# Kernel optimization log

Measured on AMD Instinct MI355X. Metric: run time of the kernel, lower is better.

Reference implementation:

```python
import jax, jax.numpy as jnp
import numpy as np

BATCH, IN, OUT = 1024, 256, 512
ALPHA = 1.0

def setup_inputs() -> dict:
    key = jax.random.key(0)
    k1, k2, k3 = jax.random.split(key, 3)
    # kaiming-uniform-ish init scale for weight, uniform bound for bias
    bound_w = 1.0 / np.sqrt(IN)
    x = jax.random.normal(k1, (BATCH, IN), dtype=jnp.float32)
    weight = jax.random.uniform(k2, (OUT, IN), dtype=jnp.float32, minval=-bound_w, maxval=bound_w)
    bias = jax.random.uniform(k3, (OUT,), dtype=jnp.float32, minval=-bound_w, maxval=bound_w)
    return {"x": x, "weight": weight, "bias": bias}

def reference(x, weight, bias):
    # assemble[b,i,o] = x[b,i] * weight[o,i]
    # this_sum[b,o]  = sum_i assemble[b,i,o]  == x @ weight.T
    this_sum = jnp.einsum('bi,oi->bo', x, weight)
    # prod over input dim of (assemble + 1)
    assemble = x[:, :, None] * weight.T[None, :, :] + 1.0  # (B, IN, OUT)
    prod = jnp.prod(assemble, axis=1)                      # (B, OUT)
    out = prod - (1.0 - ALPHA) * this_sum - 1.0 + bias
    return out
```

## Files before the change

### kernel.cpp

```cpp
#include <hip/hip_runtime.h>


#define BATCH 1024
#define IN    256
#define OUT   512

__global__ __launch_bounds__(256, 2) void product_kernel(
    const float* __restrict__ x, const float* __restrict__ w,
    const float* __restrict__ bias, float* __restrict__ out)
{
    __shared__ float4 ws4[64 * 64];

    const int tid  = threadIdx.x;
    const int wid  = tid >> 6;
    const int lane = tid & 63;
    const int sbl  = lane >> 4;
    const int l4   = lane & 15;
    const int s    = wid * 4 + sbl;

    const int o0 = blockIdx.x * 64;
    const int b0 = blockIdx.y * 16;

    const float4* x4g = (const float4*)x;
    const float4* w4g = (const float4*)w;

    #pragma unroll
    for (int it = 0; it < 16; ++it) {
        const int r = it * 4 + wid;
        ws4[r * 64 + (lane ^ ((r >> 2) & 7))] = w4g[(o0 + r) * 64 + lane];
    }
    __syncthreads();

    float4 acc[16];
    #pragma unroll
    for (int i = 0; i < 16; ++i) acc[i] = make_float4(1.0f, 1.0f, 1.0f, 1.0f);

    const int wsw = l4 & 7;
    const int wr  = 4 * l4 * 64;

    #pragma unroll 1
    for (int p = 0; p < 4; ++p) {
        const int c = 4 * s + p;

        float4 xv[16];
        #pragma unroll
        for (int i = 0; i < 16; ++i) xv[i] = x4g[(b0 + i) * 64 + c];

        const int cw = c ^ wsw;
        const float4 wv0 = ws4[wr + 0 * 64 + cw];
        const float4 wv1 = ws4[wr + 1 * 64 + cw];
        const float4 wv2 = ws4[wr + 2 * 64 + cw];
        const float4 wv3 = ws4[wr + 3 * 64 + cw];

        #pragma unroll
        for (int i = 0; i < 16; ++i) {
            acc[i].x *= __builtin_fmaf(xv[i].x, wv0.x, 1.0f);
            acc[i].y *= __builtin_fmaf(xv[i].x, wv1.x, 1.0f);
            acc[i].z *= __builtin_fmaf(xv[i].x, wv2.x, 1.0f);
            acc[i].w *= __builtin_fmaf(xv[i].x, wv3.x, 1.0f);
            acc[i].x *= __builtin_fmaf(xv[i].y, wv0.y, 1.0f);
            acc[i].y *= __builtin_fmaf(xv[i].y, wv1.y, 1.0f);
            acc[i].z *= __builtin_fmaf(xv[i].y, wv2.y, 1.0f);
            acc[i].w *= __builtin_fmaf(xv[i].y, wv3.y, 1.0f);
            acc[i].x *= __builtin_fmaf(xv[i].z, wv0.z, 1.0f);
            acc[i].y *= __builtin_fmaf(xv[i].z, wv1.z, 1.0f);
            acc[i].z *= __builtin_fmaf(xv[i].z, wv2.z, 1.0f);
            acc[i].w *= __builtin_fmaf(xv[i].z, wv3.z, 1.0f);
            acc[i].x *= __builtin_fmaf(xv[i].w, wv0.w, 1.0f);
            acc[i].y *= __builtin_fmaf(xv[i].w, wv1.w, 1.0f);
            acc[i].z *= __builtin_fmaf(xv[i].w, wv2.w, 1.0f);
            acc[i].w *= __builtin_fmaf(xv[i].w, wv3.w, 1.0f);
        }
    }

    __syncthreads();
    float4* part4 = (float4*)ws4;
    #pragma unroll
    for (int i = 0; i < 16; ++i)
        part4[(s * 16 + i) * 16 + l4] = acc[i];
    __syncthreads();

    const int r  = tid >> 4;
    const int c4 = tid & 15;
    float4 pr = part4[r * 16 + c4];
    #pragma unroll
    for (int ss = 1; ss < 16; ++ss) {
        const float4 q = part4[(ss * 16 + r) * 16 + c4];
        pr.x *= q.x; pr.y *= q.y; pr.z *= q.z; pr.w *= q.w;
    }
    const float4 bv = ((const float4*)bias)[(o0 >> 2) + c4];
    float4 o;
    o.x = pr.x - 1.0f + bv.x;
    o.y = pr.y - 1.0f + bv.y;
    o.z = pr.z - 1.0f + bv.z;
    o.w = pr.w - 1.0f + bv.w;
    ((float4*)out)[(size_t)(b0 + r) * (OUT / 4) + (o0 >> 2) + c4] = o;
}

extern "C" void kernel_launch(void* const* d_in, const int* in_sizes, int n_in,
                              void* d_out, int out_size, void* d_ws, size_t ws_size,
                              hipStream_t stream) {
    const float* x    = (const float*)d_in[0];
    const float* wgt  = (const float*)d_in[1];
    const float* bias = (const float*)d_in[2];
    float* out        = (float*)d_out;

    dim3 grid(OUT / 64, BATCH / 16);
    dim3 block(256);
    product_kernel<<<grid, block, 0, stream>>>(x, wgt, bias, out);
}
```

Baseline: 14.04 us.

## Hold weights in registers, drop LDS staging, and use packed-FMA tree products

Each thread now loads only the weight slices it needs straight from global memory into registers, so the 64 KB LDS staging of the weight tile and its barrier go away and LDS shrinks to the partial-product buffer. The inner loop uses two-wide vector FMAs and a small multiply tree (pairwise products, then a single multiply into the accumulator), which can map to packed FP32 instructions and shortens the serial multiply chain. The trade-offs are higher register pressure from the 16 weight vectors, a different floating-point product ordering, and x loads now issued inside the innermost loop.

```diff
diff --git a/kernel.cpp b/kernel.cpp
--- a/kernel.cpp
+++ b/kernel.cpp
@@ -5,11 +5,14 @@
 #define IN    256
 #define OUT   512
 
+typedef float f32x2 __attribute__((ext_vector_type(2)));
+typedef float f32x4 __attribute__((ext_vector_type(4)));
+
 __global__ __launch_bounds__(256, 2) void product_kernel(
     const float* __restrict__ x, const float* __restrict__ w,
     const float* __restrict__ bias, float* __restrict__ out)
 {
-    __shared__ float4 ws4[64 * 64];
+    __shared__ f32x4 part4[16 * 16 * 16];
 
     const int tid  = threadIdx.x;
     const int wid  = tid >> 6;
@@ -21,60 +24,43 @@
     const int o0 = blockIdx.x * 64;
     const int b0 = blockIdx.y * 16;
 
-    const float4* x4g = (const float4*)x;
-    const float4* w4g = (const float4*)w;
+    const f32x4* x4g = (const f32x4*)x;
+    const f32x4* w4g = (const f32x4*)w;
 
+    f32x4 wv[4][4];
     #pragma unroll
-    for (int it = 0; it < 16; ++it) {
-        const int r = it * 4 + wid;
-        ws4[r * 64 + (lane ^ ((r >> 2) & 7))] = w4g[(o0 + r) * 64 + lane];
-    }
-    __syncthreads();
+    for (int j = 0; j < 4; ++j)
+        #pragma unroll
+        for (int p = 0; p < 4; ++p)
+            wv[j][p] = w4g[(size_t)(o0 + 4 * l4 + j) * 64 + 4 * s + p];
 
-    float4 acc[16];
+    f32x4 acc[16];
     #pragma unroll
-    for (int i = 0; i < 16; ++i) acc[i] = make_float4(1.0f, 1.0f, 1.0f, 1.0f);
+    for (int i = 0; i < 16; ++i) acc[i] = (f32x4)(1.0f);
 
-    const int wsw = l4 & 7;
-    const int wr  = 4 * l4 * 64;
+    const f32x2 one2 = (f32x2)(1.0f);
 
     #pragma unroll 1
     for (int p = 0; p < 4; ++p) {
         const int c = 4 * s + p;
 
-        float4 xv[16];
-        #pragma unroll
-        for (int i = 0; i < 16; ++i) xv[i] = x4g[(b0 + i) * 64 + c];
-
-        const int cw = c ^ wsw;
-        const float4 wv0 = ws4[wr + 0 * 64 + cw];
-        const float4 wv1 = ws4[wr + 1 * 64 + cw];
-        const float4 wv2 = ws4[wr + 2 * 64 + cw];
-        const float4 wv3 = ws4[wr + 3 * 64 + cw];
-
         #pragma unroll
         for (int i = 0; i < 16; ++i) {
-            acc[i].x *= __builtin_fmaf(xv[i].x, wv0.x, 1.0f);
-            acc[i].y *= __builtin_fmaf(xv[i].x, wv1.x, 1.0f);
-            acc[i].z *= __builtin_fmaf(xv[i].x, wv2.x, 1.0f);
-            acc[i].w *= __builtin_fmaf(xv[i].x, wv3.x, 1.0f);
-            acc[i].x *= __builtin_fmaf(xv[i].y, wv0.y, 1.0f);
-            acc[i].y *= __builtin_fmaf(xv[i].y, wv1.y, 1.0f);
-            acc[i].z *= __builtin_fmaf(xv[i].y, wv2.y, 1.0f);
-            acc[i].w *= __builtin_fmaf(xv[i].y, wv3.y, 1.0f);
-            acc[i].x *= __builtin_fmaf(xv[i].z, wv0.z, 1.0f);
-            acc[i].y *= __builtin_fmaf(xv[i].z, wv1.z, 1.0f);
-            acc[i].z *= __builtin_fmaf(xv[i].z, wv2.z, 1.0f);
-            acc[i].w *= __builtin_fmaf(xv[i].z, wv3.z, 1.0f);
-            acc[i].x *= __builtin_fmaf(xv[i].w, wv0.w, 1.0f);
-            acc[i].y *= __builtin_fmaf(xv[i].w, wv1.w, 1.0f);
-            acc[i].z *= __builtin_fmaf(xv[i].w, wv2.w, 1.0f);
-            acc[i].w *= __builtin_fmaf(xv[i].w, wv3.w, 1.0f);
+            const f32x4 xv = x4g[(size_t)(b0 + i) * 64 + c];
+            const f32x2 xlo = __builtin_shufflevector(xv, xv, 0, 1);
+            const f32x2 xhi = __builtin_shufflevector(xv, xv, 2, 3);
+            #pragma unroll
+            for (int j = 0; j < 4; ++j) {
+                const f32x2 wlo = __builtin_shufflevector(wv[j][p], wv[j][p], 0, 1);
+                const f32x2 whi = __builtin_shufflevector(wv[j][p], wv[j][p], 2, 3);
+                const f32x2 t0 = __builtin_elementwise_fma(xlo, wlo, one2);
+                const f32x2 t1 = __builtin_elementwise_fma(xhi, whi, one2);
+                const f32x2 m  = t0 * t1;
+                acc[i][j] *= m.x * m.y;
+            }
         }
     }
 
-    __syncthreads();
-    float4* part4 = (float4*)ws4;
     #pragma unroll
     for (int i = 0; i < 16; ++i)
         part4[(s * 16 + i) * 16 + l4] = acc[i];
@@ -82,19 +68,14 @@
 
     const int r  = tid >> 4;
     const int c4 = tid & 15;
-    float4 pr = part4[r * 16 + c4];
+    f32x4 pr = part4[r * 16 + c4];
     #pragma unroll
-    for (int ss = 1; ss < 16; ++ss) {
-        const float4 q = part4[(ss * 16 + r) * 16 + c4];
-        pr.x *= q.x; pr.y *= q.y; pr.z *= q.z; pr.w *= q.w;
-    }
-    const float4 bv = ((const float4*)bias)[(o0 >> 2) + c4];
-    float4 o;
-    o.x = pr.x - 1.0f + bv.x;
-    o.y = pr.y - 1.0f + bv.y;
-    o.z = pr.z - 1.0f + bv.z;
-    o.w = pr.w - 1.0f + bv.w;
-    ((float4*)out)[(size_t)(b0 + r) * (OUT / 4) + (o0 >> 2) + c4] = o;
+    for (int ss = 1; ss < 16; ++ss)
+        pr *= part4[(ss * 16 + r) * 16 + c4];
+
+    const f32x4 bv = ((const f32x4*)bias)[(o0 >> 2) + c4];
+    const f32x4 o  = pr - 1.0f + bv;
+    ((f32x4*)out)[(size_t)(b0 + r) * (OUT / 4) + (o0 >> 2) + c4] = o;
 }
 
 extern "C" void kernel_launch(void* const* d_in, const int* in_sizes, int n_in,
```

After: 34.95 us. 149% more time.
